# Performance work log

Hardware: AMD Instinct MI355X
Metric: run time of the kernel (lower is better)

Reference implementation:

```python
import jax, jax.numpy as jnp
import numpy as np

LN_EPS = 1e-5
KERNEL_EPS = 1e-6


def setup_inputs() -> dict:
    key = jax.random.key(0)
    kx, kw, kb = jax.random.split(key, 3)
    B, N, D, H = 8, 2048, 256, 4
    x = jax.random.normal(kx, (B, N, D), dtype=jnp.float32) * 0.05
    log_sigmas = jnp.zeros((H, 1, 1), dtype=jnp.float32)
    W = jax.random.normal(kw, (D, D), dtype=jnp.float32) * 0.05  # torch Linear weight (out, in)
    b = jax.random.normal(kb, (D,), dtype=jnp.float32) * 0.05
    gamma = jnp.ones((D,), dtype=jnp.float32)
    beta = jnp.zeros((D,), dtype=jnp.float32)
    return {"x": x, "log_sigmas": log_sigmas, "W": W, "b": b, "gamma": gamma, "beta": beta}


def _layer_norm(y, gamma, beta):
    mu = jnp.mean(y, axis=-1, keepdims=True)
    var = jnp.var(y, axis=-1, keepdims=True)
    return (y - mu) * jax.lax.rsqrt(var + LN_EPS) * gamma + beta


def reference(x, log_sigmas, W, b, gamma, beta):
    # pairwise squared euclidean distances: (B, N, N)
    sq = jnp.sum(x * x, axis=-1)
    dist_sq = sq[:, :, None] + sq[:, None, :] - 2.0 * jnp.einsum('bnd,bmd->bnm', x, x)
    dist_sq = jnp.maximum(dist_sq, 0.0)
    # per-head Gaussian kernel adjacency, mean over heads
    sigmas = jnp.exp(log_sigmas)                      # (H,1,1)
    denom = 2.0 * sigmas ** 2 + KERNEL_EPS            # (H,1,1)
    adjs = jnp.exp(-dist_sq[:, None] / denom[None])   # (B,H,N,N)
    adj_final = jnp.mean(adjs, axis=1)                # (B,N,N)
    # aggregate, project, activate, residual layernorm
    out = jnp.einsum('bnm,bmd->bnd', adj_final, x)
    out = out @ W.T + b
    res = _layer_norm(jax.nn.elu(out) + x, gamma, beta)
    return res
```

## Files before the change

### kernel.cpp

```cpp
#include <hip/hip_runtime.h>

typedef unsigned short u16;
typedef __attribute__((ext_vector_type(8))) short bf16x8;
typedef __attribute__((ext_vector_type(4))) float f32x4;
typedef __attribute__((ext_vector_type(8))) unsigned short u16x8;

#define DEVI static __device__ __forceinline__

constexpr int Bb = 8, Nn = 2048, Dd = 256;

DEVI u16 f2bf(float f) {
    unsigned int u = __builtin_bit_cast(unsigned int, f);
    u = (u + 0x7fffu + ((u >> 16) & 1u)) >> 16;
    return (u16)u;
}
DEVI float bf2f(u16 v) {
    return __builtin_bit_cast(float, (unsigned int)v << 16);
}

DEVI void gl_lds16(const void* g, void* l) {
    __builtin_amdgcn_global_load_lds(
        (const __attribute__((address_space(1))) unsigned int*)g,
        (__attribute__((address_space(3))) unsigned int*)l, 16, 0, 0);
}

__global__ void prep_x_kernel(const float* __restrict__ x, u16* __restrict__ xb,
                              float* __restrict__ sq) {
    int row = blockIdx.x * 4 + (threadIdx.x >> 6);
    int l = threadIdx.x & 63;
    const float4 v = *(const float4*)(x + (size_t)row * Dd + l * 4);
    float ss = v.x * v.x + v.y * v.y + v.z * v.z + v.w * v.w;
    ushort4 o;
    o.x = f2bf(v.x); o.y = f2bf(v.y); o.z = f2bf(v.z); o.w = f2bf(v.w);
    *(ushort4*)(xb + (size_t)row * Dd + l * 4) = o;
#pragma unroll
    for (int s = 1; s < 64; s <<= 1) ss += __shfl_xor(ss, s);
    if (l == 0) sq[row] = ss;
}

__global__ void prep_w_kernel(const float* __restrict__ W, u16* __restrict__ Wb) {
    int i = (blockIdx.x * 256 + threadIdx.x) * 4;
    const float4 v = *(const float4*)(W + i);
    ushort4 o;
    o.x = f2bf(v.x); o.y = f2bf(v.y); o.z = f2bf(v.z); o.w = f2bf(v.w);
    *(ushort4*)(Wb + i) = o;
}

__global__ void prep_t_kernel(const u16* __restrict__ xb, u16* __restrict__ xbt) {
    int nt = blockIdx.x, dt = blockIdx.y, b = blockIdx.z;
    int n0 = nt * 64, d0 = dt * 64;
    __shared__ __align__(16) u16 tile[64 * 64];
    int t = threadIdx.x;
#pragma unroll
    for (int p = 0; p < 2; ++p) {
        int row = p * 32 + (t >> 3);
        int c8 = t & 7;
        uint4 v = *(const uint4*)(xb + ((size_t)(b * Nn + n0 + row)) * Dd + d0 + c8 * 8);
        *(uint4*)((char*)tile + row * 128 + ((c8 * 16) ^ ((row & 7) << 4))) = v;
    }
    __syncthreads();
#pragma unroll
    for (int p = 0; p < 2; ++p) {
        int d = p * 32 + (t >> 3);
        int nn = (t & 7) * 8;
        u16x8 vv;
#pragma unroll
        for (int e = 0; e < 8; ++e) {
            int row = nn + e;
            vv[e] = *(const u16*)((char*)tile + row * 128 + ((d * 2) ^ ((row & 7) << 4)));
        }
        *(u16x8*)(xbt + ((size_t)(b * Dd + d0 + d)) * Nn + n0 + nn) = vv;
    }
}

__global__ __launch_bounds__(512, 1) void fused_adj_kernel(
    const u16* __restrict__ xb, const u16* __restrict__ xbt,
    const float* __restrict__ sq, const float* __restrict__ lsig,
    u16* __restrict__ opart) {
    int bid = blockIdx.x;
    int xcd = bid & 7, j = bid >> 3;
    int g = xcd + 8 * (j >> 3);
    int nt8 = j & 7;
    int b = g >> 2, q = g & 3;
    int r0 = b * Nn + nt8 * 256;
    int m0b = b * Nn + q * 512;

    int tid = threadIdx.x;
    int w = tid >> 6, l = tid & 63;
    int l15 = l & 15, lhi = l >> 4;

    __shared__ __align__(16) char smem[98304];
    char* sXm = smem;
    char* sXmt = smem + 32768;
    char* sP = smem + 65536 + w * 4096;

    float nc[4];
#pragma unroll
    for (int h = 0; h < 4; ++h) {
        float denom = 2.f * expf(2.f * lsig[h]) + 1e-6f;
        nc[h] = -1.44269504f / denom;
    }
    bool uniform = (lsig[0] == lsig[1]) && (lsig[1] == lsig[2]) && (lsig[2] == lsig[3]);

    bf16x8 bf[2][8];
    float sqn[2];
#pragma unroll
    for (int rg = 0; rg < 2; ++rg) {
        const u16* xr = xb + (size_t)(r0 + w * 32 + rg * 16 + l15) * Dd;
#pragma unroll
        for (int kt = 0; kt < 8; ++kt) bf[rg][kt] = *(const bf16x8*)(xr + kt * 32 + lhi * 8);
        sqn[rg] = sq[r0 + w * 32 + rg * 16 + l15];
    }

    f32x4 of[2][16];
#pragma unroll
    for (int rg = 0; rg < 2; ++rg)
#pragma unroll
        for (int dt = 0; dt < 16; ++dt) of[rg][dt] = (f32x4){0.f, 0.f, 0.f, 0.f};

    int swz = (l15 & 7) << 4;

    for (int t = 0; t < 8; ++t) {
        int m0 = m0b + t * 64;
        __syncthreads();
#pragma unroll
        for (int it = 0; it < 4; ++it) {
            int c0 = it * 512 + w * 64;
            int c = c0 + l;
            int row = c >> 5, c16 = c & 31;
            gl_lds16(xb + (size_t)(m0 + row) * Dd + (c16 ^ (row & 7)) * 8, sXm + c0 * 16);
        }
#pragma unroll
        for (int it = 0; it < 4; ++it) {
            int c0 = it * 512 + w * 64;
            int c = c0 + l;
            int row = c >> 3, c16 = c & 7;
            gl_lds16(xbt + (size_t)(b * Dd + row) * Nn + (q * 512 + t * 64) + (c16 ^ (row & 7)) * 8,
                     sXmt + c0 * 16);
        }
        __syncthreads();

#pragma unroll
        for (int mt = 0; mt < 4; ++mt) {
            float4 sqm = *(const float4*)(sq + m0 + mt * 16 + lhi * 4);
            f32x4 sfv[2];
            sfv[0] = (f32x4){0.f, 0.f, 0.f, 0.f};
            sfv[1] = (f32x4){0.f, 0.f, 0.f, 0.f};
#pragma unroll
            for (int kt = 0; kt < 8; ++kt) {
                bf16x8 av = *(const bf16x8*)(sXm + (mt * 16 + l15) * 512 +
                                             ((kt * 64 + lhi * 16) ^ swz));
                sfv[0] = __builtin_amdgcn_mfma_f32_16x16x32_bf16(av, bf[0][kt], sfv[0], 0, 0, 0);
                sfv[1] = __builtin_amdgcn_mfma_f32_16x16x32_bf16(av, bf[1][kt], sfv[1], 0, 0, 0);
            }
            float sm[4] = {sqm.x, sqm.y, sqm.z, sqm.w};
#pragma unroll
            for (int rg = 0; rg < 2; ++rg) {
                ushort4 pk;
#pragma unroll
                for (int r = 0; r < 4; ++r) {
                    float d2 = fmaxf(fmaf(-2.f, sfv[rg][r], sqn[rg] + sm[r]), 0.f);
                    float p = exp2f(d2 * nc[0]);
                    if (!uniform)
                        p = 0.25f * (p + exp2f(d2 * nc[1]) + exp2f(d2 * nc[2]) + exp2f(d2 * nc[3]));
                    ((u16*)&pk)[r] = f2bf(p);
                }
                int n = rg * 16 + l15;
                *(ushort4*)(sP + n * 128 + ((mt * 32 + lhi * 8) ^ ((n & 7) << 4))) = pk;
            }
        }

#pragma unroll
        for (int kt2 = 0; kt2 < 2; ++kt2) {
            bf16x8 pa0 = *(const bf16x8*)(sP + l15 * 128 + ((kt2 * 64 + lhi * 16) ^ swz));
            bf16x8 pa1 = *(const bf16x8*)(sP + (16 + l15) * 128 + ((kt2 * 64 + lhi * 16) ^ swz));
#pragma unroll
            for (int dt = 0; dt < 16; ++dt) {
                bf16x8 bv = *(const bf16x8*)(sXmt + (dt * 16 + l15) * 128 +
                                             ((kt2 * 64 + lhi * 16) ^ swz));
                of[0][dt] = __builtin_amdgcn_mfma_f32_16x16x32_bf16(pa0, bv, of[0][dt], 0, 0, 0);
                of[1][dt] = __builtin_amdgcn_mfma_f32_16x16x32_bf16(pa1, bv, of[1][dt], 0, 0, 0);
            }
        }
    }

    u16* od = opart + (size_t)q * ((size_t)Bb * Nn * Dd);
#pragma unroll
    for (int rg = 0; rg < 2; ++rg)
#pragma unroll
        for (int dt = 0; dt < 16; ++dt)
#pragma unroll
            for (int r = 0; r < 4; ++r) {
                size_t row = (size_t)(r0 + w * 32 + rg * 16 + lhi * 4 + r);
                od[row * Dd + dt * 16 + l15] = f2bf(of[rg][dt][r]);
            }
}

__global__ __launch_bounds__(512, 1) void proj_ln_kernel(
    const u16* __restrict__ opart, const u16* __restrict__ Wb,
    const float* __restrict__ x, const float* __restrict__ bvec,
    const float* __restrict__ gamma, const float* __restrict__ beta,
    float* __restrict__ out) {
    int tid = threadIdx.x, w = tid >> 6, l = tid & 63;
    int rg = w & 3, h = w >> 2;
    int lrow = l & 15, lhi = l >> 4;
    size_t row0 = (size_t)blockIdx.x * 64 + rg * 16;
    const size_t QS = (size_t)Bb * Nn * Dd;

    __shared__ __align__(16) float xch[8 * 16 * 2 * 64];

    f32x4 acc[16];
#pragma unroll
    for (int jt = 0; jt < 16; ++jt) acc[jt] = (f32x4){0.f, 0.f, 0.f, 0.f};

#pragma unroll
    for (int kk = 0; kk < 4; ++kk) {
        int kc = h * 4 + kk;
        float as[8] = {0.f, 0.f, 0.f, 0.f, 0.f, 0.f, 0.f, 0.f};
#pragma unroll
        for (int qq = 0; qq < 4; ++qq) {
            u16x8 v = *(const u16x8*)(opart + QS * qq + (row0 + lrow) * Dd + kc * 32 + lhi * 8);
#pragma unroll
            for (int e = 0; e < 8; ++e) as[e] += bf2f(v[e]);
        }
        bf16x8 a;
#pragma unroll
        for (int e = 0; e < 8; ++e) a[e] = (short)f2bf(as[e]);
#pragma unroll
        for (int jt = 0; jt < 16; ++jt) {
            bf16x8 bv = *(const bf16x8*)(Wb + (size_t)(jt * 16 + lrow) * Dd + kc * 32 + lhi * 8);
            acc[jt] = __builtin_amdgcn_mfma_f32_16x16x32_bf16(a, bv, acc[jt], 0, 0, 0);
        }
    }

#pragma unroll
    for (int jt = 0; jt < 16; ++jt)
#pragma unroll
        for (int qq = 0; qq < 2; ++qq) {
            int r = (1 - h) * 2 + qq;
            xch[(w * 16 + jt) * 128 + qq * 64 + l] = acc[jt][r];
        }
    __syncthreads();
#pragma unroll
    for (int jt = 0; jt < 16; ++jt)
#pragma unroll
        for (int qq = 0; qq < 2; ++qq)
            acc[jt][h * 2 + qq] += xch[((w ^ 4) * 16 + jt) * 128 + qq * 64 + l];

#pragma unroll
    for (int qq = 0; qq < 2; ++qq) {
        int r = h * 2 + qq;
        size_t grow = row0 + lhi * 4 + r;
        float vbuf[16];
        float s1 = 0.f, s2 = 0.f;
#pragma unroll
        for (int jt = 0; jt < 16; ++jt) {
            int jcol = jt * 16 + lrow;
            float v = acc[jt][r] + bvec[jcol];
            float e = v > 0.f ? v : (exp2f(v * 1.44269504f) - 1.f);
            float res = e + x[grow * Dd + jcol];
            vbuf[jt] = res;
            s1 += res;
            s2 += res * res;
        }
#pragma unroll
        for (int m = 1; m < 16; m <<= 1) {
            s1 += __shfl_xor(s1, m);
            s2 += __shfl_xor(s2, m);
        }
        float mean = s1 * (1.f / 256.f);
        float var = s2 * (1.f / 256.f) - mean * mean;
        float rstd = rsqrtf(var + 1e-5f);
#pragma unroll
        for (int jt = 0; jt < 16; ++jt) {
            int jcol = jt * 16 + lrow;
            out[grow * Dd + jcol] = (vbuf[jt] - mean) * rstd * gamma[jcol] + beta[jcol];
        }
    }
}

extern "C" void kernel_launch(void* const* d_in, const int* in_sizes, int n_in,
                              void* d_out, int out_size, void* d_ws, size_t ws_size,
                              hipStream_t stream) {
    const float* x = (const float*)d_in[0];
    const float* lsig = (const float*)d_in[1];
    const float* W = (const float*)d_in[2];
    const float* bvec = (const float*)d_in[3];
    const float* gamma = (const float*)d_in[4];
    const float* beta = (const float*)d_in[5];
    float* out = (float*)d_out;

    char* ws = (char*)d_ws;
    u16* xb = (u16*)ws;
    u16* xbt = (u16*)(ws + 8388608);
    float* sq = (float*)(ws + 16777216);
    u16* Wb = (u16*)(ws + 16842752);
    u16* opart = (u16*)(ws + 16973824);

    prep_x_kernel<<<dim3(Bb * Nn / 4), dim3(256), 0, stream>>>(x, xb, sq);
    prep_w_kernel<<<dim3(64), dim3(256), 0, stream>>>(W, Wb);
    prep_t_kernel<<<dim3(Nn / 64, Dd / 64, Bb), dim3(256), 0, stream>>>(xb, xbt);
    fused_adj_kernel<<<dim3(256), dim3(512), 0, stream>>>(xb, xbt, sq, lsig, opart);
    proj_ln_kernel<<<dim3(Bb * Nn / 64), dim3(512), 0, stream>>>(opart, Wb, x, bvec, gamma, beta, out);
}
```

Before: 95.37 us.

## Use FP8 MFMA for distance Gram matrix and fuse prep/transpose kernels

Quantizes x to FP8 E4M3 and computes the pairwise dot products with fp8 MFMA instead of bf16, halving the LDS and register footprint of the distance stage. The bf16 conversion, sum-of-squares, FP8 packing and transpose are merged into one prep kernel, removing a separate launch and a re-read of xb. The residual in the final kernel now reads bf16 x instead of fp32. FP8 precision in the distance term can introduce large errors in exp(-d2), since x values are small (~0.05) and squared distances near zero matter, which risks correctness.

Result: slower. 104.2 us (+9.2%).

```diff
diff --git a/kernel.cpp b/kernel.cpp
--- a/kernel.cpp
+++ b/kernel.cpp
@@ -1,6 +1,7 @@
 #include <hip/hip_runtime.h>
 
 typedef unsigned short u16;
+typedef unsigned char u8;
 typedef __attribute__((ext_vector_type(8))) short bf16x8;
 typedef __attribute__((ext_vector_type(4))) float f32x4;
 typedef __attribute__((ext_vector_type(8))) unsigned short u16x8;
@@ -18,24 +19,84 @@
     return __builtin_bit_cast(float, (unsigned int)v << 16);
 }
 
+DEVI unsigned f2e4m3(float f) {
+    unsigned u = __builtin_bit_cast(unsigned, f);
+    unsigned s = (u >> 24) & 0x80u;
+    int e = (int)((u >> 23) & 0xffu) - 127;
+    unsigned m = u & 0x7fffffu;
+    if (e >= -6) {
+        if (e >= 8) return s | 0x7eu;
+        unsigned m3 = m >> 20;
+        unsigned rest = m & 0xfffffu;
+        m3 += (rest > 0x80000u) || ((rest == 0x80000u) && (m3 & 1u));
+        return s | (((unsigned)(e + 7) << 3) + m3);
+    }
+    if (e >= -9) {
+        unsigned full = 0x800000u | m;
+        int shift = 23 - (e + 9);
+        unsigned qv = full >> shift;
+        unsigned rest = full & ((1u << shift) - 1u);
+        unsigned half = 1u << (shift - 1);
+        qv += (rest > half) || ((rest == half) && (qv & 1u));
+        return s | qv;
+    }
+    if (e == -10 && m != 0) return s | 1u;
+    return s;
+}
+
 DEVI void gl_lds16(const void* g, void* l) {
     __builtin_amdgcn_global_load_lds(
         (const __attribute__((address_space(1))) unsigned int*)g,
         (__attribute__((address_space(3))) unsigned int*)l, 16, 0, 0);
 }
 
-__global__ void prep_x_kernel(const float* __restrict__ x, u16* __restrict__ xb,
-                              float* __restrict__ sq) {
-    int row = blockIdx.x * 4 + (threadIdx.x >> 6);
-    int l = threadIdx.x & 63;
-    const float4 v = *(const float4*)(x + (size_t)row * Dd + l * 4);
-    float ss = v.x * v.x + v.y * v.y + v.z * v.z + v.w * v.w;
-    ushort4 o;
-    o.x = f2bf(v.x); o.y = f2bf(v.y); o.z = f2bf(v.z); o.w = f2bf(v.w);
-    *(ushort4*)(xb + (size_t)row * Dd + l * 4) = o;
-#pragma unroll
-    for (int s = 1; s < 64; s <<= 1) ss += __shfl_xor(ss, s);
-    if (l == 0) sq[row] = ss;
+__global__ __launch_bounds__(256) void prep_xt_kernel(
+    const float* __restrict__ x, u16* __restrict__ xb, u16* __restrict__ xbt,
+    u8* __restrict__ x8, float* __restrict__ sq) {
+    int n0 = blockIdx.x * 64;
+    int b = blockIdx.y;
+    int t = threadIdx.x;
+    __shared__ __align__(16) u16 tile[64 * 256];
+    int row = t >> 2;
+    int c0 = (t & 3) * 64;
+    size_t gr = (size_t)(b * Nn + n0 + row);
+    const float* xr = x + gr * Dd + c0;
+    u16* xbr = xb + gr * Dd + c0;
+    float ss = 0.f;
+    unsigned wpk[16];
+#pragma unroll
+    for (int cc = 0; cc < 16; ++cc) {
+        float4 v = *(const float4*)(xr + cc * 4);
+        ss += v.x * v.x + v.y * v.y + v.z * v.z + v.w * v.w;
+        ushort4 o;
+        o.x = f2bf(v.x); o.y = f2bf(v.y); o.z = f2bf(v.z); o.w = f2bf(v.w);
+        *(ushort4*)(xbr + cc * 4) = o;
+        int cb = (c0 + cc * 4) * 2;
+        *(ushort4*)((char*)tile + row * 512 + (cb ^ ((row & 7) << 4))) = o;
+        wpk[cc] = f2e4m3(v.x) | (f2e4m3(v.y) << 8) | (f2e4m3(v.z) << 16) | (f2e4m3(v.w) << 24);
+    }
+#pragma unroll
+    for (int k = 0; k < 4; ++k) {
+        uint4 pw;
+        pw.x = wpk[k * 4]; pw.y = wpk[k * 4 + 1]; pw.z = wpk[k * 4 + 2]; pw.w = wpk[k * 4 + 3];
+        *(uint4*)(x8 + gr * 256 + c0 + k * 16) = pw;
+    }
+    ss += __shfl_xor(ss, 1);
+    ss += __shfl_xor(ss, 2);
+    if ((t & 3) == 0) sq[gr] = ss;
+    __syncthreads();
+#pragma unroll
+    for (int p = 0; p < 8; ++p) {
+        int d = p * 32 + (t >> 3);
+        int n8 = (t & 7) * 8;
+        u16x8 vv;
+#pragma unroll
+        for (int e = 0; e < 8; ++e) {
+            int r2 = n8 + e;
+            vv[e] = *(const u16*)((char*)tile + r2 * 512 + ((d * 2) ^ ((r2 & 7) << 4)));
+        }
+        *(u16x8*)(xbt + ((size_t)(b * Dd + d)) * Nn + n0 + n8) = vv;
+    }
 }
 
 __global__ void prep_w_kernel(const float* __restrict__ W, u16* __restrict__ Wb) {
@@ -46,35 +107,8 @@
     *(ushort4*)(Wb + i) = o;
 }
 
-__global__ void prep_t_kernel(const u16* __restrict__ xb, u16* __restrict__ xbt) {
-    int nt = blockIdx.x, dt = blockIdx.y, b = blockIdx.z;
-    int n0 = nt * 64, d0 = dt * 64;
-    __shared__ __align__(16) u16 tile[64 * 64];
-    int t = threadIdx.x;
-#pragma unroll
-    for (int p = 0; p < 2; ++p) {
-        int row = p * 32 + (t >> 3);
-        int c8 = t & 7;
-        uint4 v = *(const uint4*)(xb + ((size_t)(b * Nn + n0 + row)) * Dd + d0 + c8 * 8);
-        *(uint4*)((char*)tile + row * 128 + ((c8 * 16) ^ ((row & 7) << 4))) = v;
-    }
-    __syncthreads();
-#pragma unroll
-    for (int p = 0; p < 2; ++p) {
-        int d = p * 32 + (t >> 3);
-        int nn = (t & 7) * 8;
-        u16x8 vv;
-#pragma unroll
-        for (int e = 0; e < 8; ++e) {
-            int row = nn + e;
-            vv[e] = *(const u16*)((char*)tile + row * 128 + ((d * 2) ^ ((row & 7) << 4)));
-        }
-        *(u16x8*)(xbt + ((size_t)(b * Dd + d0 + d)) * Nn + n0 + nn) = vv;
-    }
-}
-
 __global__ __launch_bounds__(512, 1) void fused_adj_kernel(
-    const u16* __restrict__ xb, const u16* __restrict__ xbt,
+    const u8* __restrict__ x8, const u16* __restrict__ xbt,
     const float* __restrict__ sq, const float* __restrict__ lsig,
     u16* __restrict__ opart) {
     int bid = blockIdx.x;
@@ -84,15 +118,16 @@
     int b = g >> 2, q = g & 3;
     int r0 = b * Nn + nt8 * 256;
     int m0b = b * Nn + q * 512;
+    int mq0 = q * 512;
 
     int tid = threadIdx.x;
     int w = tid >> 6, l = tid & 63;
     int l15 = l & 15, lhi = l >> 4;
 
-    __shared__ __align__(16) char smem[98304];
-    char* sXm = smem;
-    char* sXmt = smem + 32768;
-    char* sP = smem + 65536 + w * 4096;
+    __shared__ __align__(16) char smem[81920];
+    char* sXm8 = smem;
+    char* sXmt = smem + 16384;
+    char* sP = smem + 49152 + w * 4096;
 
     float nc[4];
 #pragma unroll
@@ -102,13 +137,13 @@
     }
     bool uniform = (lsig[0] == lsig[1]) && (lsig[1] == lsig[2]) && (lsig[2] == lsig[3]);
 
-    bf16x8 bf[2][8];
+    long bf8[2][8];
     float sqn[2];
 #pragma unroll
     for (int rg = 0; rg < 2; ++rg) {
-        const u16* xr = xb + (size_t)(r0 + w * 32 + rg * 16 + l15) * Dd;
-#pragma unroll
-        for (int kt = 0; kt < 8; ++kt) bf[rg][kt] = *(const bf16x8*)(xr + kt * 32 + lhi * 8);
+        const u8* xr = x8 + (size_t)(r0 + w * 32 + rg * 16 + l15) * 256;
+#pragma unroll
+        for (int kt = 0; kt < 8; ++kt) bf8[rg][kt] = *(const long*)(xr + kt * 32 + lhi * 8);
         sqn[rg] = sq[r0 + w * 32 + rg * 16 + l15];
     }
 
@@ -124,18 +159,18 @@
         int m0 = m0b + t * 64;
         __syncthreads();
 #pragma unroll
-        for (int it = 0; it < 4; ++it) {
-            int c0 = it * 512 + w * 64;
-            int c = c0 + l;
-            int row = c >> 5, c16 = c & 31;
-            gl_lds16(xb + (size_t)(m0 + row) * Dd + (c16 ^ (row & 7)) * 8, sXm + c0 * 16);
+        for (int it = 0; it < 2; ++it) {
+            int c = w * 2 + it;
+            int row = c * 4 + (l >> 4);
+            gl_lds16(x8 + (size_t)(m0 + row) * 256 + (((l & 15) * 16) ^ ((row & 7) << 4)),
+                     sXm8 + c * 1024);
         }
 #pragma unroll
         for (int it = 0; it < 4; ++it) {
             int c0 = it * 512 + w * 64;
             int c = c0 + l;
             int row = c >> 3, c16 = c & 7;
-            gl_lds16(xbt + (size_t)(b * Dd + row) * Nn + (q * 512 + t * 64) + (c16 ^ (row & 7)) * 8,
+            gl_lds16(xbt + (size_t)(b * Dd + row) * Nn + (mq0 + t * 64) + (c16 ^ (row & 7)) * 8,
                      sXmt + c0 * 16);
         }
         __syncthreads();
@@ -143,23 +178,23 @@
 #pragma unroll
         for (int mt = 0; mt < 4; ++mt) {
             float4 sqm = *(const float4*)(sq + m0 + mt * 16 + lhi * 4);
-            f32x4 sfv[2];
-            sfv[0] = (f32x4){0.f, 0.f, 0.f, 0.f};
-            sfv[1] = (f32x4){0.f, 0.f, 0.f, 0.f};
+            f32x4 sfv0 = (f32x4){0.f, 0.f, 0.f, 0.f};
+            f32x4 sfv1 = (f32x4){0.f, 0.f, 0.f, 0.f};
 #pragma unroll
             for (int kt = 0; kt < 8; ++kt) {
-                bf16x8 av = *(const bf16x8*)(sXm + (mt * 16 + l15) * 512 +
-                                             ((kt * 64 + lhi * 16) ^ swz));
-                sfv[0] = __builtin_amdgcn_mfma_f32_16x16x32_bf16(av, bf[0][kt], sfv[0], 0, 0, 0);
-                sfv[1] = __builtin_amdgcn_mfma_f32_16x16x32_bf16(av, bf[1][kt], sfv[1], 0, 0, 0);
+                long av = *(const long*)(sXm8 + (mt * 16 + l15) * 256 +
+                                         ((kt * 32 + lhi * 8) ^ swz));
+                sfv0 = __builtin_amdgcn_mfma_f32_16x16x32_fp8_fp8(av, bf8[0][kt], sfv0, 0, 0, 0);
+                sfv1 = __builtin_amdgcn_mfma_f32_16x16x32_fp8_fp8(av, bf8[1][kt], sfv1, 0, 0, 0);
             }
             float sm[4] = {sqm.x, sqm.y, sqm.z, sqm.w};
 #pragma unroll
             for (int rg = 0; rg < 2; ++rg) {
+                f32x4 sfv = rg ? sfv1 : sfv0;
                 ushort4 pk;
 #pragma unroll
                 for (int r = 0; r < 4; ++r) {
-                    float d2 = fmaxf(fmaf(-2.f, sfv[rg][r], sqn[rg] + sm[r]), 0.f);
+                    float d2 = fmaxf(fmaf(-2.f, sfv[r], sqn[rg] + sm[r]), 0.f);
                     float p = exp2f(d2 * nc[0]);
                     if (!uniform)
                         p = 0.25f * (p + exp2f(d2 * nc[1]) + exp2f(d2 * nc[2]) + exp2f(d2 * nc[3]));
@@ -198,7 +233,7 @@
 
 __global__ __launch_bounds__(512, 1) void proj_ln_kernel(
     const u16* __restrict__ opart, const u16* __restrict__ Wb,
-    const float* __restrict__ x, const float* __restrict__ bvec,
+    const u16* __restrict__ xbres, const float* __restrict__ bvec,
     const float* __restrict__ gamma, const float* __restrict__ beta,
     float* __restrict__ out) {
     int tid = threadIdx.x, w = tid >> 6, l = tid & 63;
@@ -258,7 +293,7 @@
             int jcol = jt * 16 + lrow;
             float v = acc[jt][r] + bvec[jcol];
             float e = v > 0.f ? v : (exp2f(v * 1.44269504f) - 1.f);
-            float res = e + x[grow * Dd + jcol];
+            float res = e + bf2f(xbres[grow * Dd + jcol]);
             vbuf[jt] = res;
             s1 += res;
             s2 += res * res;
@@ -295,11 +330,11 @@
     u16* xbt = (u16*)(ws + 8388608);
     float* sq = (float*)(ws + 16777216);
     u16* Wb = (u16*)(ws + 16842752);
-    u16* opart = (u16*)(ws + 16973824);
-
-    prep_x_kernel<<<dim3(Bb * Nn / 4), dim3(256), 0, stream>>>(x, xb, sq);
+    u8* x8 = (u8*)(ws + 16973824);
+    u16* opart = (u16*)(ws + 21168128);
+
+    prep_xt_kernel<<<dim3(Nn / 64, Bb), dim3(256), 0, stream>>>(x, xb, xbt, x8, sq);
     prep_w_kernel<<<dim3(64), dim3(256), 0, stream>>>(W, Wb);
-    prep_t_kernel<<<dim3(Nn / 64, Dd / 64, Bb), dim3(256), 0, stream>>>(xb, xbt);
-    fused_adj_kernel<<<dim3(256), dim3(512), 0, stream>>>(xb, xbt, sq, lsig, opart);
-    proj_ln_kernel<<<dim3(Bb * Nn / 64), dim3(512), 0, stream>>>(opart, Wb, x, bvec, gamma, beta, out);
-}
+    fused_adj_kernel<<<dim3(256), dim3(512), 0, stream>>>(x8, xbt, sq, lsig, opart);
+    proj_ln_kernel<<<dim3(Bb * Nn / 64), dim3(512), 0, stream>>>(opart, Wb, xb, bvec, gamma, beta, out);
+}
```
